# Kernel tuning notes

Hardware: AMD Instinct MI355X
Metric: run time of the kernel (lower is better)

Reference implementation:

```python
import jax, jax.numpy as jnp
from jax import lax
import numpy as np

B, L, D, H, E, NL = 32, 512, 1024, 256, 64, 3


def _rev_within(x_tm, lens):
    # reverse each sequence within its own length; x_tm: (L, B, ...)
    t = jnp.arange(x_tm.shape[0])[:, None]                      # (L,1)
    idx = jnp.where(t < lens[None, :], lens[None, :] - 1 - t, t)  # (L,B)
    return jnp.take_along_axis(x_tm, idx[:, :, None], axis=0)


def _lstm_dir(x_tm, lens, w_ih, w_hh, b, reverse):
    # x_tm: (L,B,Din); w_ih: (4H,Din); w_hh: (4H,H); b: (4H,)
    Lx, Bx, _ = x_tm.shape
    Hh = w_hh.shape[1]
    if reverse:
        x_tm = _rev_within(x_tm, lens)
    xg = jnp.einsum('lbd,gd->lbg', x_tm, w_ih) + b              # (L,B,4H)

    def step(carry, xg_t):
        h, c = carry
        g = xg_t + h @ w_hh.T
        i, f, gg, o = jnp.split(g, 4, axis=-1)
        c = jax.nn.sigmoid(f) * c + jax.nn.sigmoid(i) * jnp.tanh(gg)
        h = jax.nn.sigmoid(o) * jnp.tanh(c)
        return (h, c), h

    z = jnp.zeros((Bx, Hh), x_tm.dtype)
    _, hs = lax.scan(step, (z, z), xg)
    if reverse:
        hs = _rev_within(hs, lens)
    return hs


def _bilstm(x, lens, w_ih_l0, w_hh_l0, b_l0, w_ih_l12, w_hh_l12, b_l12):
    # x: (B,L,D) -> time-major (L,B,D)
    h = jnp.transpose(x, (1, 0, 2))
    valid = (jnp.arange(h.shape[0])[:, None] < lens[None, :]).astype(x.dtype)  # (L,B)
    wi = [w_ih_l0] + [w_ih_l12[i] for i in range(w_ih_l12.shape[0])]
    wh = [w_hh_l0] + [w_hh_l12[i] for i in range(w_hh_l12.shape[0])]
    bb = [b_l0] + [b_l12[i] for i in range(b_l12.shape[0])]
    for li in range(len(wi)):
        f = _lstm_dir(h, lens, wi[li][0], wh[li][0], bb[li][0], False)
        bwd = _lstm_dir(h, lens, wi[li][1], wh[li][1], bb[li][1], True)
        # pad_packed_sequence zeros padded positions
        h = jnp.concatenate([f, bwd], axis=-1) * valid[:, :, None]
    return h  # (L,B,2H)


def _crf_loss(out_tm, tags, mask, lens, fc_w, fc_b, trans):
    xb = jnp.transpose(out_tm, (1, 0, 2))                       # (B,L,2H)
    emit = jax.nn.softmax(xb @ fc_w.T + fc_b, axis=2)           # (B,L,E)
    valid = 1.0 - mask.astype(emit.dtype)                       # (B,L), 1=real token
    sc = jnp.take_along_axis(emit, tags[:, :, None], axis=2)[..., 0]
    sc = sc.at[:, 1:].add(trans[tags[:, :-1], tags[:, 1:]])
    total = (sc * valid).sum(axis=1)                            # (B,)

    emit_t = jnp.transpose(emit, (1, 0, 2))                     # (L,B,E)
    valid_t = valid.T                                           # (L,B)

    def step(d, inp):
        e_t, v_t = inp
        # d_new[b,j] = logsumexp_k(d[b,k] + trans[k,j]) + emit[b,t,j]
        d_new = jax.scipy.special.logsumexp(d[:, :, None] + trans[None], axis=1) + e_t
        return jnp.where(v_t[:, None] > 0, d_new, d), None

    d, _ = lax.scan(step, emit_t[0], (emit_t[1:], valid_t[1:]))
    Z = jax.scipy.special.logsumexp(d, axis=1)                  # (B,)
    loss = -(total - Z) / valid.sum(axis=1)                     # normalize by length
    return loss.mean()


def setup_inputs() -> dict:
    key = jax.random.key(0)
    ks = jax.random.split(key, 12)
    x = jax.random.normal(ks[0], (B, L, D), dtype=jnp.float32)
    lens = jnp.sort(jax.random.randint(ks[1], (B,), 1, L + 1))[::-1]
    lens = lens.at[0].set(L)
    mask = jnp.arange(L)[None, :] >= lens[:, None]              # True = padding
    tags = jax.random.randint(ks[2], (B, L), 0, E)
    s0 = 1.0 / np.sqrt(H)
    w_ih_l0 = jax.random.uniform(ks[3], (2, 4 * H, D), minval=-s0, maxval=s0)
    w_hh_l0 = jax.random.uniform(ks[4], (2, 4 * H, H), minval=-s0, maxval=s0)
    b_l0 = jax.random.uniform(ks[5], (2, 4 * H), minval=-s0, maxval=s0)
    w_ih_l12 = jax.random.uniform(ks[6], (2, 2, 4 * H, 2 * H), minval=-s0, maxval=s0)
    w_hh_l12 = jax.random.uniform(ks[7], (2, 2, 4 * H, H), minval=-s0, maxval=s0)
    b_l12 = jax.random.uniform(ks[8], (2, 2, 4 * H), minval=-s0, maxval=s0)
    fc_w = jax.random.normal(ks[9], (E, 2 * H)) * 0.02
    fc_b = jnp.zeros((E,), jnp.float32)
    trans = jax.random.normal(ks[10], (E, E))
    return {"x": x, "lens": lens, "tags": tags, "mask": mask,
            "w_ih_l0": w_ih_l0, "w_hh_l0": w_hh_l0, "b_l0": b_l0,
            "w_ih_l12": w_ih_l12, "w_hh_l12": w_hh_l12, "b_l12": b_l12,
            "fc_w": fc_w, "fc_b": fc_b, "trans": trans}


def reference(x, lens, tags, mask, w_ih_l0, w_hh_l0, b_l0,
              w_ih_l12, w_hh_l12, b_l12, fc_w, fc_b, trans):
    out = _bilstm(x, lens, w_ih_l0, w_hh_l0, b_l0, w_ih_l12, w_hh_l12, b_l12)
    return _crf_loss(out, tags, mask, lens, fc_w, fc_b, trans)
```

## Files before the change

kernel.cpp:

```cpp
#include <hip/hip_runtime.h>
#include <hip/hip_fp16.h>

#define Bb 32
#define Ll 512
#define Dd 1024
#define Hh 256
#define Ee 64

__device__ __forceinline__ float sigmoidf_(float x) { return 1.f / (1.f + __expf(-x)); }
__device__ __forceinline__ float tanhf_(float x) { return 1.f - 2.f / (__expf(2.f * x) + 1.f); }

typedef _Float16 v8hf __attribute__((ext_vector_type(8)));
typedef float v4f __attribute__((ext_vector_type(4)));

__device__ __forceinline__ int sdot8_(unsigned int a, unsigned int b, int acc) {
#if __has_builtin(__builtin_amdgcn_sdot8)
  return __builtin_amdgcn_sdot8((int)a, (int)b, acc, false);
#else
  int r = acc;
#pragma unroll
  for (int i = 0; i < 8; i++)
    r += (((int)(a << (28 - 4 * i))) >> 28) * (((int)(b << (28 - 4 * i))) >> 28);
  return r;
#endif
}

__device__ __forceinline__ void dot8c(uint4 wv, uint4 hv, int& a, int& b) {
  a = sdot8_(wv.x, hv.x, a);
  b = sdot8_(wv.y, hv.y, b);
  a = sdot8_(wv.z, hv.z, a);
  b = sdot8_(wv.w, hv.w, b);
}

__global__ __launch_bounds__(256) void cvt_h(const float* __restrict__ s,
                                             __half* __restrict__ d, int n8) {
  const int i = blockIdx.x * 256 + threadIdx.x;
  if (i >= n8) return;
  const float4 a = ((const float4*)s)[2 * i];
  const float4 b = ((const float4*)s)[2 * i + 1];
  union { __half h[8]; uint4 u; } o;
  o.h[0] = __float2half(a.x); o.h[1] = __float2half(a.y);
  o.h[2] = __float2half(a.z); o.h[3] = __float2half(a.w);
  o.h[4] = __float2half(b.x); o.h[5] = __float2half(b.y);
  o.h[6] = __float2half(b.z); o.h[7] = __float2half(b.w);
  ((uint4*)d)[i] = o.u;
}

__global__ __launch_bounds__(256) void conv_wq2(const float* __restrict__ src,
                                                uint4* __restrict__ dst) {
  const int s = blockIdx.y;
  const int idx = blockIdx.x * 256 + threadIdx.x;
  const int row = idx & 1023;
  const int ch = idx >> 10;
  const float* sp = src + (size_t)s * 262144 + (size_t)row * 256 + ch * 32;
  unsigned int u[4];
#pragma unroll
  for (int d = 0; d < 4; ++d) {
    unsigned int dw = 0;
#pragma unroll
    for (int n = 0; n < 8; ++n) {
      int q = (int)rintf(sp[d * 8 + n] * 112.f);
      q = max(-7, min(7, q));
      dw |= ((unsigned int)(q & 0xF)) << (4 * n);
    }
    u[d] = dw;
  }
  dst[(size_t)s * 8192 + (size_t)ch * 1024 + row] = make_uint4(u[0], u[1], u[2], u[3]);
}

template <int DK, bool XL>
__global__ __launch_bounds__(512) void xg_gemm2(const __half* __restrict__ A,
                                                const __half* __restrict__ W,
                                                const float* __restrict__ bias,
                                                __half* __restrict__ xg) {
  const int dir = blockIdx.x >> 3;
  const int n0 = (blockIdx.x & 7) * 128;
  const int m0 = blockIdx.y * 128;
  const __half* Wd = W + (size_t)dir * (1024 * DK);
  const float* bd = bias + dir * 1024;
  __half* out = xg + (size_t)dir * (16384ull * 1024);

  __shared__ __align__(16) __half As[128][40];
  __shared__ __align__(16) __half Bs[128][40];

  const int tid = threadIdx.x;
  const int wave = tid >> 6, lane = tid & 63;
  const int wr = wave >> 2, wc = wave & 3;
  const int fr = lane & 15, kg = lane >> 4;

  v4f acc[4][2];
#pragma unroll
  for (int i = 0; i < 4; i++)
#pragma unroll
    for (int jj = 0; jj < 2; jj++) acc[i][jj] = (v4f)(0.f);

  const int lr = tid >> 2;
  const int lc = (tid & 3) * 8;
  size_t abase;
  if (XL) {
    const int m = m0 + lr, t = m >> 5, bb = m & 31;
    abase = ((size_t)(bb * 512 + t)) * DK + lc;
  } else {
    abase = (size_t)(m0 + lr) * DK + lc;
  }
  const size_t bbase = (size_t)(n0 + lr) * DK + lc;

  for (int k0 = 0; k0 < DK; k0 += 32) {
    *(uint4*)&As[lr][lc] = *(const uint4*)(A + abase + k0);
    *(uint4*)&Bs[lr][lc] = *(const uint4*)(Wd + bbase + k0);
    __syncthreads();
    v8hf af[4], bf[2];
#pragma unroll
    for (int i = 0; i < 4; i++)
      af[i] = *(const v8hf*)&As[wr * 64 + i * 16 + fr][kg * 8];
#pragma unroll
    for (int jj = 0; jj < 2; jj++)
      bf[jj] = *(const v8hf*)&Bs[wc * 32 + jj * 16 + fr][kg * 8];
#pragma unroll
    for (int i = 0; i < 4; i++)
#pragma unroll
      for (int jj = 0; jj < 2; jj++)
        acc[i][jj] = __builtin_amdgcn_mfma_f32_16x16x32_f16(af[i], bf[jj], acc[i][jj], 0, 0, 0);
    __syncthreads();
  }

#pragma unroll
  for (int jj = 0; jj < 2; jj++) {
    const int n = n0 + wc * 32 + jj * 16 + fr;
    const float bv = bd[n];
#pragma unroll
    for (int i = 0; i < 4; i++) {
#pragma unroll
      for (int r = 0; r < 4; ++r) {
        const int m = m0 + wr * 64 + i * 16 + kg * 4 + r;
        out[(size_t)m * 1024 + n] = __float2half(acc[i][jj][r] + bv);
      }
    }
  }
}

__global__ __launch_bounds__(512, 1) void lstm_layer15(const uint4* __restrict__ WQ2,
                                                       const __half* __restrict__ xg,
                                                       const int* __restrict__ lens,
                                                       __half* __restrict__ out) {
  const int w = blockIdx.x, dir = w >> 5, b = w & 31;
  const int tid = threadIdx.x, gh = tid >> 8, j = tid & 255;
  const int row0 = (2 * gh) * 256 + j;
  const int row1 = row0 + 256;

  __shared__ __align__(16) uint4 Wc[2 * 1024];
  __shared__ __align__(16) uint4 hq4[2][8];
  __shared__ __align__(16) float aex[2][256];

  const uint4* __restrict__ Wt = WQ2 + (size_t)dir * 8192;

#pragma unroll
  for (int i = 0; i < 4; ++i)
    Wc[i * 512 + tid] = Wt[i * 512 + tid];

  uint4 sw0[6], sw1[6];
#pragma unroll
  for (int ch = 0; ch < 6; ++ch) {
    sw0[ch] = Wt[(size_t)(2 + ch) * 1024 + row0];
    sw1[ch] = Wt[(size_t)(2 + ch) * 1024 + row1];
  }

  if (tid < 32) ((unsigned int*)&hq4[0][0])[tid] = 0u;
  const int mylen = lens[b];
  float c = 0.f;

  const __half* xgb = xg + (size_t)dir * (512ull * 32 * 1024) + (size_t)b * 1024 + j;
  int tt = dir ? (mylen - 1) : 0;
  float p0, p1;
  {
    const __half* xr = xgb + (size_t)tt * (32 * 1024);
    p0 = __half2float(xr[(2 * gh) * 256]);
    p1 = __half2float(xr[(2 * gh + 1) * 256]);
  }
  __syncthreads();

#pragma unroll 1
  for (int t = 0; t < 512; ++t) {
    const int tcur = tt;
    const uint4* hp = &hq4[t & 1][0];
    int A0 = 0, B0 = 0, A1 = 0, B1 = 0;

#pragma unroll
    for (int ch = 0; ch < 2; ++ch) {
      const uint4 hv = hp[ch];
      dot8c(Wc[ch * 1024 + row0], hv, A0, B0);
      dot8c(Wc[ch * 1024 + row1], hv, A1, B1);
    }
#pragma unroll
    for (int ch = 0; ch < 6; ++ch) {
      const uint4 hv = hp[2 + ch];
      dot8c(sw0[ch], hv, A0, B0);
      dot8c(sw1[ch], hv, A1, B1);
    }

    const float sc = 1.2755102e-3f;
    const float a0 = (float)(A0 + B0) * sc + p0;
    const float a1 = (float)(A1 + B1) * sc + p1;

    if (gh == 1) {
      aex[0][j] = tanhf_(a0);
      aex[1][j] = sigmoidf_(a1);
    }
    __syncthreads();
    if (gh == 0) {
      const float ig = sigmoidf_(a0);
      const float fg = sigmoidf_(a1);
      c = fg * c + ig * aex[0][j];
      const float hnew = aex[1][j] * tanhf_(c);
      out[((size_t)tcur * 32 + b) * 512 + dir * 256 + j] =
          __float2half((tcur < mylen) ? hnew : 0.f);
      const int q = (int)rintf(hnew * 7.f);
      const int pk = __shfl_xor(q, 1);
      if ((j & 1) == 0)
        ((unsigned char*)&hq4[(t + 1) & 1][0])[j >> 1] =
            (unsigned char)((q & 0xF) | ((pk & 0xF) << 4));
    }
    if (t < 511) {
      const int tn = t + 1;
      tt = dir ? ((tn < mylen) ? (mylen - 1 - tn) : tn) : tn;
      const __half* xr = xgb + (size_t)tt * (32 * 1024);
      p0 = __half2float(xr[(2 * gh) * 256]);
      p1 = __half2float(xr[(2 * gh + 1) * 256]);
    }
    __syncthreads();
  }
}

__global__ __launch_bounds__(256) void emit_gemm(const __half* __restrict__ outA,
                                                 const __half* __restrict__ fcwh,
                                                 const float* __restrict__ fcb,
                                                 float* __restrict__ emit) {
  const int m0 = blockIdx.x * 64;
  __shared__ __align__(16) __half As[64][40];
  __shared__ __align__(16) __half Bs[64][40];

  const int tid = threadIdx.x;
  const int wave = tid >> 6, lane = tid & 63;
  const int fr = lane & 15, kg = lane >> 4;

  v4f acc[4];
#pragma unroll
  for (int i = 0; i < 4; i++) acc[i] = (v4f)(0.f);

  const int lr = tid >> 2;
  const int lc = (tid & 3) * 8;
  const size_t abase = (size_t)(m0 + lr) * 512 + lc;
  const size_t bbase = (size_t)lr * 512 + lc;

  for (int k0 = 0; k0 < 512; k0 += 32) {
    *(uint4*)&As[lr][lc] = *(const uint4*)(outA + abase + k0);
    *(uint4*)&Bs[lr][lc] = *(const uint4*)(fcwh + bbase + k0);
    __syncthreads();
    const v8hf af = *(const v8hf*)&As[wave * 16 + fr][kg * 8];
#pragma unroll
    for (int nb = 0; nb < 4; ++nb) {
      const v8hf bf = *(const v8hf*)&Bs[nb * 16 + fr][kg * 8];
      acc[nb] = __builtin_amdgcn_mfma_f32_16x16x32_f16(af, bf, acc[nb], 0, 0, 0);
    }
    __syncthreads();
  }

  float bv[4];
#pragma unroll
  for (int nb = 0; nb < 4; ++nb) bv[nb] = fcb[nb * 16 + fr];

#pragma unroll
  for (int r = 0; r < 4; ++r) {
    float v0 = acc[0][r] + bv[0], v1 = acc[1][r] + bv[1];
    float v2 = acc[2][r] + bv[2], v3 = acc[3][r] + bv[3];
    float mx = fmaxf(fmaxf(v0, v1), fmaxf(v2, v3));
#pragma unroll
    for (int off = 8; off; off >>= 1) mx = fmaxf(mx, __shfl_xor(mx, off));
    const float e0 = __expf(v0 - mx), e1 = __expf(v1 - mx);
    const float e2 = __expf(v2 - mx), e3 = __expf(v3 - mx);
    float sm = (e0 + e1) + (e2 + e3);
#pragma unroll
    for (int off = 8; off; off >>= 1) sm += __shfl_xor(sm, off);
    const float rinv = 1.f / sm;
    const int mrow = m0 + wave * 16 + kg * 4 + r;
    const int bb = mrow & 31, ttt = mrow >> 5;
    float* ep = emit + ((size_t)bb * 512 + ttt) * 64;
    ep[0 * 16 + fr] = e0 * rinv;
    ep[1 * 16 + fr] = e1 * rinv;
    ep[2 * 16 + fr] = e2 * rinv;
    ep[3 * 16 + fr] = e3 * rinv;
  }
}

__global__ __launch_bounds__(256) void score_kernel(const float* __restrict__ emit,
                                                    const float* __restrict__ trans,
                                                    const int* __restrict__ tags,
                                                    const int* __restrict__ lens,
                                                    float* __restrict__ total) {
  const int b = blockIdx.x;
  const int len = lens[b];
  float part = 0.f;
  for (int t = threadIdx.x; t < len; t += 256) {
    const int tg = tags[b * Ll + t];
    float v = emit[((size_t)b * Ll + t) * Ee + tg];
    if (t >= 1) v += trans[tags[b * Ll + t - 1] * Ee + tg];
    part += v;
  }
  for (int off = 32; off; off >>= 1) part += __shfl_xor(part, off);
  __shared__ float wsum[4];
  if ((threadIdx.x & 63) == 0) wsum[threadIdx.x >> 6] = part;
  __syncthreads();
  if (threadIdx.x == 0) total[b] = wsum[0] + wsum[1] + wsum[2] + wsum[3];
}

__global__ __launch_bounds__(64) void crf_prep(const float* __restrict__ trans,
                                               float* __restrict__ E,
                                               float* __restrict__ cm) {
  const int j = threadIdx.x;
  float m = -1e30f;
  for (int k = 0; k < 64; k++) m = fmaxf(m, trans[k * 64 + j]);
  cm[j] = m;
  for (int k = 0; k < 64; k++) E[j * 64 + k] = __expf(trans[k * 64 + j] - m);
}

__global__ __launch_bounds__(64) void crf_scan2(const float* __restrict__ emit,
                                                const float* __restrict__ E,
                                                const float* __restrict__ cm,
                                                const int* __restrict__ lens,
                                                float* __restrict__ dout) {
  const int b = blockIdx.x, j = threadIdx.x;
  __shared__ float el[2][64];
  float Er[64];
#pragma unroll
  for (int kc = 0; kc < 16; ++kc) {
    const float4 v = *(const float4*)(E + j * 64 + 4 * kc);
    Er[4 * kc + 0] = v.x; Er[4 * kc + 1] = v.y;
    Er[4 * kc + 2] = v.z; Er[4 * kc + 3] = v.w;
  }
  const float cmj = cm[j];
  const int len = lens[b];
  const float* eb = emit + (size_t)b * 512 * 64 + j;
  float d = eb[0];
  float enext = (len > 1) ? eb[64] : 0.f;

  for (int t = 1; t < len; ++t) {
    float m = d;
#pragma unroll
    for (int off = 32; off; off >>= 1) m = fmaxf(m, __shfl_xor(m, off));
    const float ej = __expf(d - m);
    el[t & 1][j] = ej;
    const float emt = enext;
    if (t + 1 < len) enext = eb[(size_t)(t + 1) * 64];
    __syncthreads();
    float s0 = 0.f, s1 = 0.f, s2 = 0.f, s3 = 0.f;
    const float4* e4 = (const float4*)&el[t & 1][0];
#pragma unroll
    for (int kc = 0; kc < 16; ++kc) {
      const float4 ev = e4[kc];
      s0 = fmaf(ev.x, Er[4 * kc + 0], s0);
      s1 = fmaf(ev.y, Er[4 * kc + 1], s1);
      s2 = fmaf(ev.z, Er[4 * kc + 2], s2);
      s3 = fmaf(ev.w, Er[4 * kc + 3], s3);
    }
    d = __logf((s0 + s1) + (s2 + s3)) + m + cmj + emt;
    __syncthreads();
  }
  dout[b * 64 + j] = d;
}

__global__ __launch_bounds__(64) void final_kernel(const float* __restrict__ dbuf,
                                                   const float* __restrict__ total,
                                                   const int* __restrict__ lens,
                                                   float* __restrict__ out) {
  const int j = threadIdx.x;
  float lsum = 0.f;
  for (int b = 0; b < 32; b++) {
    const float d = dbuf[b * 64 + j];
    float m = d;
    for (int off = 32; off; off >>= 1) m = fmaxf(m, __shfl_xor(m, off));
    const float e = __expf(d - m);
    float s = e;
    for (int off = 32; off; off >>= 1) s += __shfl_xor(s, off);
    const float Z = __logf(s) + m;
    if (j == 0) lsum += -(total[b] - Z) / (float)lens[b];
  }
  if (j == 0) out[0] = lsum / 32.f;
}

extern "C" void kernel_launch(void* const* d_in, const int* in_sizes, int n_in,
                              void* d_out, int out_size, void* d_ws, size_t ws_size,
                              hipStream_t stream) {
  const float* x = (const float*)d_in[0];
  const int* lens = (const int*)d_in[1];
  const int* tags = (const int*)d_in[2];
  const float* w_ih_l0 = (const float*)d_in[4];
  const float* w_hh_l0 = (const float*)d_in[5];
  const float* b_l0 = (const float*)d_in[6];
  const float* w_ih_l12 = (const float*)d_in[7];
  const float* w_hh_l12 = (const float*)d_in[8];
  const float* b_l12 = (const float*)d_in[9];
  const float* fc_w = (const float*)d_in[10];
  const float* fc_b = (const float*)d_in[11];
  const float* trans = (const float*)d_in[12];

  char* ws = (char*)d_ws;
  __half* xg = (__half*)ws;
  __half* xh = (__half*)(ws + 67108864);
  __half* outA = (__half*)(ws + 100663296);
  __half* outB = (__half*)(ws + 117440512);
  uint4* WQ2 = (uint4*)(ws + 134217728);
  __half* WIH0 = (__half*)(ws + 137363456);
  __half* WIH12 = (__half*)(ws + 141557760);
  float* Ebuf = (float*)(ws + 145752064);
  float* cmbuf = (float*)(ws + 145768448);
  __half* fcwh = (__half*)(ws + 145768960);
  float* emit = (float*)ws;
  float* total = (float*)(ws + 4194304);
  float* dbuf = total + 32;

  cvt_h<<<8192, 256, 0, stream>>>(x, xh, 2097152);
  cvt_h<<<1024, 256, 0, stream>>>(w_ih_l0, WIH0, 262144);
  cvt_h<<<1024, 256, 0, stream>>>(w_ih_l12, WIH12, 262144);
  cvt_h<<<16, 256, 0, stream>>>(fc_w, fcwh, 4096);
  conv_wq2<<<dim3(32, 2), 256, 0, stream>>>(w_hh_l0, WQ2);
  conv_wq2<<<dim3(32, 4), 256, 0, stream>>>(w_hh_l12, WQ2 + 2 * 8192);
  crf_prep<<<1, 64, 0, stream>>>(trans, Ebuf, cmbuf);

  const dim3 ggrid(16, 128);

  xg_gemm2<1024, true><<<ggrid, 512, 0, stream>>>(xh, WIH0, b_l0, xg);
  lstm_layer15<<<64, 512, 0, stream>>>(WQ2, xg, lens, outA);

  xg_gemm2<512, false><<<ggrid, 512, 0, stream>>>(outA, WIH12, b_l12, xg);
  lstm_layer15<<<64, 512, 0, stream>>>(WQ2 + 2 * 8192, xg, lens, outB);

  xg_gemm2<512, false><<<ggrid, 512, 0, stream>>>(outB, WIH12 + 2 * 1024 * 512,
                                                  b_l12 + 2 * 1024, xg);
  lstm_layer15<<<64, 512, 0, stream>>>(WQ2 + 4 * 8192, xg, lens, outA);

  emit_gemm<<<256, 256, 0, stream>>>(outA, fcwh, fc_b, emit);
  score_kernel<<<Bb, 256, 0, stream>>>(emit, trans, tags, lens, total);
  crf_scan2<<<Bb, 64, 0, stream>>>(emit, Ebuf, cmbuf, lens, dbuf);
  final_kernel<<<1, 64, 0, stream>>>(dbuf, total, lens, (float*)d_out);
}
```

Baseline: 2.065 ms.

## Split LSTM recurrence over K halves with wave shuffle, drop mid-step barrier

Reorganizes the LSTM step kernel so that each thread computes all four gates for one hidden unit over half of the K dimension. The two K halves live in the two half-waves and are combined with a cross-lane shuffle. This removes the shared-memory gate exchange and the second __syncthreads per timestep, leaving one barrier per step. More weights now sit in LDS (four chunks instead of two) and per-thread register weights are rearranged to match. In exchange each step does extra shuffles and more LDS reads, and every thread evaluates all four activations.

```diff
diff --git a/kernel.cpp b/kernel.cpp
--- a/kernel.cpp
+++ b/kernel.cpp
@@ -139,31 +139,36 @@
   }
 }
 
-__global__ __launch_bounds__(512, 1) void lstm_layer15(const uint4* __restrict__ WQ2,
+__global__ __launch_bounds__(512, 1) void lstm_layer16(const uint4* __restrict__ WQ2,
                                                        const __half* __restrict__ xg,
                                                        const int* __restrict__ lens,
                                                        __half* __restrict__ out) {
   const int w = blockIdx.x, dir = w >> 5, b = w & 31;
-  const int tid = threadIdx.x, gh = tid >> 8, j = tid & 255;
-  const int row0 = (2 * gh) * 256 + j;
-  const int row1 = row0 + 256;
-
-  __shared__ __align__(16) uint4 Wc[2 * 1024];
+  const int tid = threadIdx.x;
+  const int wv = tid >> 6, lane = tid & 63;
+  const int kh = lane >> 5;
+  const int j = wv * 32 + (lane & 31);
+
+  __shared__ __align__(16) uint4 Wc[4 * 1024];
   __shared__ __align__(16) uint4 hq4[2][8];
-  __shared__ __align__(16) float aex[2][256];
 
   const uint4* __restrict__ Wt = WQ2 + (size_t)dir * 8192;
 
 #pragma unroll
-  for (int i = 0; i < 4; ++i)
-    Wc[i * 512 + tid] = Wt[i * 512 + tid];
-
-  uint4 sw0[6], sw1[6];
-#pragma unroll
-  for (int ch = 0; ch < 6; ++ch) {
-    sw0[ch] = Wt[(size_t)(2 + ch) * 1024 + row0];
-    sw1[ch] = Wt[(size_t)(2 + ch) * 1024 + row1];
-  }
+  for (int i = 0; i < 8; ++i) {
+    const int pos = i * 512 + tid;
+    const int cc = pos >> 10;
+    const int rr = pos & 1023;
+    const int src = (cc < 2) ? cc : cc + 2;
+    Wc[pos] = Wt[(size_t)src * 1024 + rr];
+  }
+
+  uint4 sw[2][4];
+#pragma unroll
+  for (int s = 0; s < 2; ++s)
+#pragma unroll
+    for (int g = 0; g < 4; ++g)
+      sw[s][g] = Wt[(size_t)(kh * 4 + 2 + s) * 1024 + g * 256 + j];
 
   if (tid < 32) ((unsigned int*)&hq4[0][0])[tid] = 0u;
   const int mylen = lens[b];
@@ -171,11 +176,11 @@
 
   const __half* xgb = xg + (size_t)dir * (512ull * 32 * 1024) + (size_t)b * 1024 + j;
   int tt = dir ? (mylen - 1) : 0;
-  float p0, p1;
+  float p0, p1, p2, p3;
   {
     const __half* xr = xgb + (size_t)tt * (32 * 1024);
-    p0 = __half2float(xr[(2 * gh) * 256]);
-    p1 = __half2float(xr[(2 * gh + 1) * 256]);
+    p0 = __half2float(xr[0]);   p1 = __half2float(xr[256]);
+    p2 = __half2float(xr[512]); p3 = __half2float(xr[768]);
   }
   __syncthreads();
 
@@ -183,49 +188,70 @@
   for (int t = 0; t < 512; ++t) {
     const int tcur = tt;
     const uint4* hp = &hq4[t & 1][0];
+    uint4 hv0 = hp[kh * 4 + 0];
+    uint4 hv1 = hp[kh * 4 + 1];
+    uint4 hv2 = hp[kh * 4 + 2];
+    uint4 hv3 = hp[kh * 4 + 3];
+
     int A0 = 0, B0 = 0, A1 = 0, B1 = 0;
-
-#pragma unroll
-    for (int ch = 0; ch < 2; ++ch) {
-      const uint4 hv = hp[ch];
-      dot8c(Wc[ch * 1024 + row0], hv, A0, B0);
-      dot8c(Wc[ch * 1024 + row1], hv, A1, B1);
-    }
-#pragma unroll
-    for (int ch = 0; ch < 6; ++ch) {
-      const uint4 hv = hp[2 + ch];
-      dot8c(sw0[ch], hv, A0, B0);
-      dot8c(sw1[ch], hv, A1, B1);
-    }
+    int A2 = 0, B2 = 0, A3 = 0, B3 = 0;
+
+    {
+      const uint4* wb = &Wc[(kh * 2) * 1024 + j];
+      dot8c(wb[0], hv0, A0, B0);
+      dot8c(wb[256], hv0, A1, B1);
+      dot8c(wb[512], hv0, A2, B2);
+      dot8c(wb[768], hv0, A3, B3);
+      const uint4* wb1 = &Wc[(kh * 2 + 1) * 1024 + j];
+      dot8c(wb1[0], hv1, A0, B0);
+      dot8c(wb1[256], hv1, A1, B1);
+      dot8c(wb1[512], hv1, A2, B2);
+      dot8c(wb1[768], hv1, A3, B3);
+    }
+    dot8c(sw[0][0], hv2, A0, B0);
+    dot8c(sw[0][1], hv2, A1, B1);
+    dot8c(sw[0][2], hv2, A2, B2);
+    dot8c(sw[0][3], hv2, A3, B3);
+    dot8c(sw[1][0], hv3, A0, B0);
+    dot8c(sw[1][1], hv3, A1, B1);
+    dot8c(sw[1][2], hv3, A2, B2);
+    dot8c(sw[1][3], hv3, A3, B3);
+
+    int t0 = A0 + B0, t1 = A1 + B1, t2 = A2 + B2, t3 = A3 + B3;
+    t0 += __shfl_xor(t0, 32);
+    t1 += __shfl_xor(t1, 32);
+    t2 += __shfl_xor(t2, 32);
+    t3 += __shfl_xor(t3, 32);
 
     const float sc = 1.2755102e-3f;
-    const float a0 = (float)(A0 + B0) * sc + p0;
-    const float a1 = (float)(A1 + B1) * sc + p1;
-
-    if (gh == 1) {
-      aex[0][j] = tanhf_(a0);
-      aex[1][j] = sigmoidf_(a1);
-    }
-    __syncthreads();
-    if (gh == 0) {
-      const float ig = sigmoidf_(a0);
-      const float fg = sigmoidf_(a1);
-      c = fg * c + ig * aex[0][j];
-      const float hnew = aex[1][j] * tanhf_(c);
+    const float a0 = (float)t0 * sc + p0;
+    const float a1 = (float)t1 * sc + p1;
+    const float a2 = (float)t2 * sc + p2;
+    const float a3 = (float)t3 * sc + p3;
+
+    const float ig = sigmoidf_(a0);
+    const float fg = sigmoidf_(a1);
+    const float gg = tanhf_(a2);
+    const float og = sigmoidf_(a3);
+    c = fg * c + ig * gg;
+    const float hnew = og * tanhf_(c);
+
+    const int q = (int)rintf(hnew * 7.f);
+    const int pk = __shfl_xor(q, 1);
+    if (kh == 0) {
       out[((size_t)tcur * 32 + b) * 512 + dir * 256 + j] =
           __float2half((tcur < mylen) ? hnew : 0.f);
-      const int q = (int)rintf(hnew * 7.f);
-      const int pk = __shfl_xor(q, 1);
       if ((j & 1) == 0)
         ((unsigned char*)&hq4[(t + 1) & 1][0])[j >> 1] =
             (unsigned char)((q & 0xF) | ((pk & 0xF) << 4));
     }
+
     if (t < 511) {
       const int tn = t + 1;
       tt = dir ? ((tn < mylen) ? (mylen - 1 - tn) : tn) : tn;
       const __half* xr = xgb + (size_t)tt * (32 * 1024);
-      p0 = __half2float(xr[(2 * gh) * 256]);
-      p1 = __half2float(xr[(2 * gh + 1) * 256]);
+      p0 = __half2float(xr[0]);   p1 = __half2float(xr[256]);
+      p2 = __half2float(xr[512]); p3 = __half2float(xr[768]);
     }
     __syncthreads();
   }
@@ -429,14 +455,14 @@
   const dim3 ggrid(16, 128);
 
   xg_gemm2<1024, true><<<ggrid, 512, 0, stream>>>(xh, WIH0, b_l0, xg);
-  lstm_layer15<<<64, 512, 0, stream>>>(WQ2, xg, lens, outA);
+  lstm_layer16<<<64, 512, 0, stream>>>(WQ2, xg, lens, outA);
 
   xg_gemm2<512, false><<<ggrid, 512, 0, stream>>>(outA, WIH12, b_l12, xg);
-  lstm_layer15<<<64, 512, 0, stream>>>(WQ2 + 2 * 8192, xg, lens, outB);
+  lstm_layer16<<<64, 512, 0, stream>>>(WQ2 + 2 * 8192, xg, lens, outB);
 
   xg_gemm2<512, false><<<ggrid, 512, 0, stream>>>(outB, WIH12 + 2 * 1024 * 512,
                                                   b_l12 + 2 * 1024, xg);
-  lstm_layer15<<<64, 512, 0, stream>>>(WQ2 + 4 * 8192, xg, lens, outA);
+  lstm_layer16<<<64, 512, 0, stream>>>(WQ2 + 4 * 8192, xg, lens, outA);
 
   emit_gemm<<<256, 256, 0, stream>>>(outA, fcwh, fc_b, emit);
   score_kernel<<<Bb, 256, 0, stream>>>(emit, trans, tags, lens, total);
```

Measured after the change: 2.271 ms. 9.9% more time.

## Compute all four LSTM gates per thread, removing mid-step barrier

Applied to the files above, without the earlier changes.

The recurrent LSTM kernel drops from 512 to 256 threads per block, so each thread now computes all four gate dot products for one hidden unit. This removes the shared-memory exchange of tanh/sigmoid values and the extra __syncthreads inside every timestep. More of the quantized recurrent weights now sit in LDS (3 of 8 chunks instead of 2), and the rest stay in registers (5 chunks of 4 gates). The trade is double the dot-product work per thread on the serial critical path, plus higher register pressure.

```diff
diff --git a/kernel.cpp b/kernel.cpp
--- a/kernel.cpp
+++ b/kernel.cpp
@@ -139,43 +139,40 @@
   }
 }
 
-__global__ __launch_bounds__(512, 1) void lstm_layer15(const uint4* __restrict__ WQ2,
+__global__ __launch_bounds__(256, 1) void lstm_layer17(const uint4* __restrict__ WQ2,
                                                        const __half* __restrict__ xg,
                                                        const int* __restrict__ lens,
                                                        __half* __restrict__ out) {
   const int w = blockIdx.x, dir = w >> 5, b = w & 31;
-  const int tid = threadIdx.x, gh = tid >> 8, j = tid & 255;
-  const int row0 = (2 * gh) * 256 + j;
-  const int row1 = row0 + 256;
-
-  __shared__ __align__(16) uint4 Wc[2 * 1024];
+  const int j = threadIdx.x;
+
+  __shared__ __align__(16) uint4 Wc[3 * 1024];
   __shared__ __align__(16) uint4 hq4[2][8];
-  __shared__ __align__(16) float aex[2][256];
 
   const uint4* __restrict__ Wt = WQ2 + (size_t)dir * 8192;
 
 #pragma unroll
-  for (int i = 0; i < 4; ++i)
-    Wc[i * 512 + tid] = Wt[i * 512 + tid];
-
-  uint4 sw0[6], sw1[6];
-#pragma unroll
-  for (int ch = 0; ch < 6; ++ch) {
-    sw0[ch] = Wt[(size_t)(2 + ch) * 1024 + row0];
-    sw1[ch] = Wt[(size_t)(2 + ch) * 1024 + row1];
-  }
-
-  if (tid < 32) ((unsigned int*)&hq4[0][0])[tid] = 0u;
+  for (int i = 0; i < 12; ++i)
+    Wc[i * 256 + j] = Wt[i * 256 + j];
+
+  uint4 sw[5][4];
+#pragma unroll
+  for (int ch = 0; ch < 5; ++ch)
+#pragma unroll
+    for (int g = 0; g < 4; ++g)
+      sw[ch][g] = Wt[(size_t)(3 + ch) * 1024 + g * 256 + j];
+
+  if (j < 32) ((unsigned int*)&hq4[0][0])[j] = 0u;
   const int mylen = lens[b];
   float c = 0.f;
 
   const __half* xgb = xg + (size_t)dir * (512ull * 32 * 1024) + (size_t)b * 1024 + j;
   int tt = dir ? (mylen - 1) : 0;
-  float p0, p1;
+  float p0, p1, p2, p3;
   {
     const __half* xr = xgb + (size_t)tt * (32 * 1024);
-    p0 = __half2float(xr[(2 * gh) * 256]);
-    p1 = __half2float(xr[(2 * gh + 1) * 256]);
+    p0 = __half2float(xr[0]);   p1 = __half2float(xr[256]);
+    p2 = __half2float(xr[512]); p3 = __half2float(xr[768]);
   }
   __syncthreads();
 
@@ -183,49 +180,57 @@
   for (int t = 0; t < 512; ++t) {
     const int tcur = tt;
     const uint4* hp = &hq4[t & 1][0];
+    uint4 hv[8];
+#pragma unroll
+    for (int ch = 0; ch < 8; ++ch) hv[ch] = hp[ch];
+
     int A0 = 0, B0 = 0, A1 = 0, B1 = 0;
-
-#pragma unroll
-    for (int ch = 0; ch < 2; ++ch) {
-      const uint4 hv = hp[ch];
-      dot8c(Wc[ch * 1024 + row0], hv, A0, B0);
-      dot8c(Wc[ch * 1024 + row1], hv, A1, B1);
-    }
-#pragma unroll
-    for (int ch = 0; ch < 6; ++ch) {
-      const uint4 hv = hp[2 + ch];
-      dot8c(sw0[ch], hv, A0, B0);
-      dot8c(sw1[ch], hv, A1, B1);
+    int A2 = 0, B2 = 0, A3 = 0, B3 = 0;
+
+#pragma unroll
+    for (int ch = 0; ch < 3; ++ch) {
+      const uint4* wb = &Wc[ch * 1024 + j];
+      dot8c(wb[0], hv[ch], A0, B0);
+      dot8c(wb[256], hv[ch], A1, B1);
+      dot8c(wb[512], hv[ch], A2, B2);
+      dot8c(wb[768], hv[ch], A3, B3);
+    }
+#pragma unroll
+    for (int ch = 0; ch < 5; ++ch) {
+      const uint4 h4 = hv[3 + ch];
+      dot8c(sw[ch][0], h4, A0, B0);
+      dot8c(sw[ch][1], h4, A1, B1);
+      dot8c(sw[ch][2], h4, A2, B2);
+      dot8c(sw[ch][3], h4, A3, B3);
     }
 
     const float sc = 1.2755102e-3f;
     const float a0 = (float)(A0 + B0) * sc + p0;
     const float a1 = (float)(A1 + B1) * sc + p1;
-
-    if (gh == 1) {
-      aex[0][j] = tanhf_(a0);
-      aex[1][j] = sigmoidf_(a1);
-    }
-    __syncthreads();
-    if (gh == 0) {
-      const float ig = sigmoidf_(a0);
-      const float fg = sigmoidf_(a1);
-      c = fg * c + ig * aex[0][j];
-      const float hnew = aex[1][j] * tanhf_(c);
-      out[((size_t)tcur * 32 + b) * 512 + dir * 256 + j] =
-          __float2half((tcur < mylen) ? hnew : 0.f);
-      const int q = (int)rintf(hnew * 7.f);
-      const int pk = __shfl_xor(q, 1);
-      if ((j & 1) == 0)
-        ((unsigned char*)&hq4[(t + 1) & 1][0])[j >> 1] =
-            (unsigned char)((q & 0xF) | ((pk & 0xF) << 4));
-    }
+    const float a2 = (float)(A2 + B2) * sc + p2;
+    const float a3 = (float)(A3 + B3) * sc + p3;
+
+    const float ig = sigmoidf_(a0);
+    const float fg = sigmoidf_(a1);
+    const float gg = tanhf_(a2);
+    const float og = sigmoidf_(a3);
+    c = fg * c + ig * gg;
+    const float hnew = og * tanhf_(c);
+
+    out[((size_t)tcur * 32 + b) * 512 + dir * 256 + j] =
+        __float2half((tcur < mylen) ? hnew : 0.f);
+    const int q = (int)rintf(hnew * 7.f);
+    const int pk = __shfl_xor(q, 1);
+    if ((j & 1) == 0)
+      ((unsigned char*)&hq4[(t + 1) & 1][0])[j >> 1] =
+          (unsigned char)((q & 0xF) | ((pk & 0xF) << 4));
+
     if (t < 511) {
       const int tn = t + 1;
       tt = dir ? ((tn < mylen) ? (mylen - 1 - tn) : tn) : tn;
       const __half* xr = xgb + (size_t)tt * (32 * 1024);
-      p0 = __half2float(xr[(2 * gh) * 256]);
-      p1 = __half2float(xr[(2 * gh + 1) * 256]);
+      p0 = __half2float(xr[0]);   p1 = __half2float(xr[256]);
+      p2 = __half2float(xr[512]); p3 = __half2float(xr[768]);
     }
     __syncthreads();
   }
@@ -429,14 +434,14 @@
   const dim3 ggrid(16, 128);
 
   xg_gemm2<1024, true><<<ggrid, 512, 0, stream>>>(xh, WIH0, b_l0, xg);
-  lstm_layer15<<<64, 512, 0, stream>>>(WQ2, xg, lens, outA);
+  lstm_layer17<<<64, 256, 0, stream>>>(WQ2, xg, lens, outA);
 
   xg_gemm2<512, false><<<ggrid, 512, 0, stream>>>(outA, WIH12, b_l12, xg);
-  lstm_layer15<<<64, 512, 0, stream>>>(WQ2 + 2 * 8192, xg, lens, outB);
+  lstm_layer17<<<64, 256, 0, stream>>>(WQ2 + 2 * 8192, xg, lens, outB);
 
   xg_gemm2<512, false><<<ggrid, 512, 0, stream>>>(outB, WIH12 + 2 * 1024 * 512,
                                                   b_l12 + 2 * 1024, xg);
-  lstm_layer15<<<64, 512, 0, stream>>>(WQ2 + 4 * 8192, xg, lens, outA);
+  lstm_layer17<<<64, 256, 0, stream>>>(WQ2 + 4 * 8192, xg, lens, outA);
 
   emit_gemm<<<256, 256, 0, stream>>>(outA, fcwh, fc_b, emit);
   score_kernel<<<Bb, 256, 0, stream>>>(emit, trans, tags, lens, total);
```

After: 2.081 ms. Within noise of the previous version (+0.8%).
